# Optimization experiments

Hardware: AMD Instinct MI355X
Metric: run time of the kernel (lower is better)

## Reference

```python
import jax, jax.numpy as jnp
import numpy as np

B, L, S, H = 8, 128, 160, 768      # batch, words, wordpieces, bert hidden
T, CD = 16, 50                      # max chars per word, char embed/lstm dim
WV, WD = 50000, 100                 # word vocab, word embed dim
CV = 128                            # char vocab
NEG = -1e30


def _run_lstm(x, w_ih, w_hh, b):
    # x: [N, T, D] -> hidden states [N, T, Hc]; torch LSTM gate order i,f,g,o
    N = x.shape[0]
    Hc = w_hh.shape[1]
    def step(carry, xt):
        h, c = carry
        g = xt @ w_ih.T + h @ w_hh.T + b
        i, f, gg, o = jnp.split(g, 4, axis=-1)
        c = jax.nn.sigmoid(f) * c + jax.nn.sigmoid(i) * jnp.tanh(gg)
        h = jax.nn.sigmoid(o) * jnp.tanh(c)
        return (h, c), h
    init = (jnp.zeros((N, Hc), x.dtype), jnp.zeros((N, Hc), x.dtype))
    _, hs = jax.lax.scan(step, init, jnp.swapaxes(x, 0, 1))
    return jnp.swapaxes(hs, 0, 1)


def setup_inputs() -> dict:
    key = jax.random.key(0)
    ks = jax.random.split(key, 14)
    sc = 1.0 / np.sqrt(CD)
    return {
        "bert_emb": jax.random.normal(ks[0], (B, S, H), jnp.float32),
        "pieces2word": jax.random.randint(ks[1], (B, L, S), 0, 2, jnp.int32),
        "word_ids": jax.random.randint(ks[2], (B, L), 0, WV),
        "char_ids": jax.random.randint(ks[3], (B, L, T), 0, CV),
        "char_count": jax.random.randint(ks[4], (B, L), 0, T, jnp.int32),
        "token_masks_char": jax.random.randint(ks[5], (B, L, T), 0, 2, jnp.int32),
        "word_table": jax.random.normal(ks[6], (WV, WD), jnp.float32) * 0.02,
        "char_table": jax.random.normal(ks[7], (CV, CD), jnp.float32) * 0.02,
        "w_ih_f": jax.random.uniform(ks[8], (4 * CD, CD), jnp.float32, -sc, sc),
        "w_hh_f": jax.random.uniform(ks[9], (4 * CD, CD), jnp.float32, -sc, sc),
        "b_f": jax.random.uniform(ks[10], (4 * CD,), jnp.float32, -sc, sc),
        "w_ih_b": jax.random.uniform(ks[11], (4 * CD, CD), jnp.float32, -sc, sc),
        "w_hh_b": jax.random.uniform(ks[12], (4 * CD, CD), jnp.float32, -sc, sc),
        "b_b": jax.random.uniform(ks[13], (4 * CD,), jnp.float32, -sc, sc),
    }


def reference(bert_emb, pieces2word, word_ids, char_ids, char_count,
              token_masks_char, word_table, char_table,
              w_ih_f, w_hh_f, b_f, w_ih_b, w_hh_b, b_b):
    cls_embedding = bert_emb[:, 0]                      # [B, H]
    # piece -> word max pooling (masked fill with global min, then max)
    min_value = jax.lax.stop_gradient(jnp.min(bert_emb))
    expanded = jnp.where(pieces2word[:, :, :, None] != 0,
                         bert_emb[:, None, :, :], min_value)  # [B, L, S, H]
    word_reps = jnp.max(expanded, axis=2)               # [B, L, H]

    # word embedding lookup (emb_dropout is identity in eval)
    word_embed = word_table[word_ids]                   # [B, L, WD]

    # char biLSTM
    N = B * L
    lengths = jnp.maximum(char_count.reshape(N), 1)     # char_count[==0] = 1
    x = char_table[char_ids.reshape(N, T)]              # [N, T, CD]
    h_fwd = _run_lstm(x, w_ih_f, w_hh_f, b_f)           # [N, T, CD]
    # reverse each sequence by its true length (packed-sequence semantics)
    t = jnp.arange(T)
    rev_idx = lengths[:, None] - 1 - t[None, :]         # [N, T]
    valid = (rev_idx >= 0).astype(x.dtype)[:, :, None]
    gidx = jnp.clip(rev_idx, 0, T - 1)[:, :, None]
    x_rev = jnp.take_along_axis(x, gidx, axis=1) * valid
    h_rev = _run_lstm(x_rev, w_ih_b, w_hh_b, b_b)
    h_bwd = jnp.take_along_axis(h_rev, gidx, axis=1) * valid  # un-reverse + zero pad
    char_h = jnp.concatenate([h_fwd, h_bwd], axis=-1).reshape(B, L, T, 2 * CD)

    # combine(..., 'max'): additive -1e30 mask, max over chars, zero all-masked
    m = jnp.where(token_masks_char[:, :, :, None] == 0, NEG, 0.0).astype(char_h.dtype)
    h_token_char = jnp.max(m + char_h, axis=2)
    h_token_char = jnp.where(h_token_char == NEG, 0.0, h_token_char)  # [B, L, 2CD]

    embeds = jnp.concatenate([word_reps, word_embed, h_token_char], axis=-1)
    return embeds, cls_embedding
```

## Files before the change

kernel.cpp:

```cpp
#include <hip/hip_runtime.h>

#define B_   8
#define L_   128
#define S_   160
#define H_   768
#define T_   16
#define CD_  50
#define WD_  100
#define NGATE 200
#define NEGV (-1e30f)
#define FMAXV 3.402823466e+38f
#define NELEM (B_ * S_ * H_)

typedef short  s16x8 __attribute__((ext_vector_type(8)));
typedef float  f32x4 __attribute__((ext_vector_type(4)));

__device__ __forceinline__ unsigned short f2bf(float f) {
    unsigned u = __float_as_uint(f);
    u = (u + 0x7FFFu + ((u >> 16) & 1u)) >> 16;
    return (unsigned short)u;
}
__device__ __forceinline__ float sigm(float x) {
    return __fdividef(1.f, 1.f + __expf(-x));
}
__device__ __forceinline__ float tanh_fast(float x) {
    float a = fabsf(x);
    float e = __expf(-2.f * a);
    float t = __fdividef(1.f - e, 1.f + e);
    return copysignf(t, x);
}
__device__ __forceinline__ float4 fmax4(float4 a, float4 b) {
    return make_float4(fmaxf(a.x, b.x), fmaxf(a.y, b.y), fmaxf(a.z, b.z), fmaxf(a.w, b.w));
}

struct LstmS {
    s16x8 xall[T_][128];
    s16x8 hbuf[2][128];
    int   slen[16], smask[16];
};
struct WordS {
    int list[S_ + 8];
    int cnt;
    float red[256];
};
#define SMEM_BYTES 37120

__device__ void lstm_body(int unit, char* smem,
        const int* __restrict__ char_ids, const int* __restrict__ char_count,
        const int* __restrict__ tok_mask, const float* __restrict__ char_table,
        const float* __restrict__ w_ih_f, const float* __restrict__ w_hh_f,
        const float* __restrict__ b_f,
        const float* __restrict__ w_ih_b, const float* __restrict__ w_hh_b,
        const float* __restrict__ b_b,
        float* __restrict__ out) {
    LstmS& sh = *(LstmS*)smem;
    const int dir  = unit >> 6;
    const int grp  = unit & 63;
    const int tid  = threadIdx.x;
    const int lane = tid & 63;
    const int wv   = tid >> 6;

    if (tid < 16) {
        int n = grp * 16 + tid;
        int c = char_count[n];
        sh.slen[tid] = (c > 0) ? c : 1;
        int mb = 0;
        for (int t = 0; t < T_; ++t) mb |= (tok_mask[n * T_ + t] != 0) << t;
        sh.smask[tid] = mb;
    }
    { s16x8 z = {0,0,0,0,0,0,0,0};
      if (tid < 128) sh.hbuf[0][tid] = z; else sh.hbuf[1][tid - 128] = z; }

    const int m   = lane & 3;
    const int k2  = (lane >> 2) & 3;
    const int q   = lane >> 4;
    const int sstar = q * 4 + m;

    const float* WI = dir ? w_ih_b : w_ih_f;
    const float* WH = dir ? w_hh_b : w_hh_f;
    const float* BV = dir ? b_b    : b_f;
    const int cnt = (wv == 0) ? 4 : 3;
    int   ccol[4];
    int   cvld[4];
    int   hofs[4];
    s16x8 bf[4][4];
#pragma unroll
    for (int i = 0; i < 4; ++i) {
        int nt = (i < 3) ? (wv + 4 * i) : 12;
        int c  = nt * 4 + k2;
        int jv = (i < cnt) && (c < 50);
        ccol[i] = c;
        cvld[i] = jv;
        hofs[i] = ((c >> 3) * 16 + sstar) * 8 + (c & 7);
        int orow = m * 50 + c;
        const float* wi = WI + orow * CD_;
        const float* wh = WH + orow * CD_;
#pragma unroll
        for (int kt = 0; kt < 4; ++kt) {
            int kst = kt * 32 + q * 8;
            s16x8 fr = {0,0,0,0,0,0,0,0};
#pragma unroll
            for (int e = 0; e < 8; ++e) {
                int k = kst + e;
                float v = 0.f;
                if (jv) {
                    if (k < 64) {
                        if (k < CD_) v = wi[k];
                        else if (k == 63) v = BV[orow];
                    } else {
                        int kk = k - 64;
                        if (kk < CD_) v = wh[kk];
                    }
                }
                fr[e] = (short)f2bf(v);
            }
            bf[i][kt] = fr;
        }
    }
    __syncthreads();

    for (int idx = tid; idx < T_ * 128; idx += 256) {
        int t = idx >> 7;
        int u = idx & 127;
        int g = u >> 4, s = u & 15;
        int st = dir ? (sh.slen[s] - 1 - t) : t;
        s16x8 fr = {0,0,0,0,0,0,0,0};
        if (st >= 0) {
            int cidv = char_ids[(grp * 16 + s) * T_ + st];
            const float* row = char_table + cidv * CD_;
            int kbase = g * 8;
#pragma unroll
            for (int e = 0; e < 8; ++e) {
                int k = kbase + e;
                if (k < CD_) fr[e] = (short)f2bf(row[k]);
            }
        }
        if (g == 7) fr[7] = (short)0x3F80;
        sh.xall[t][u] = fr;
    }

    const int laneofs = (q << 4) + (lane & 15);
    const int sl_s = sh.slen[sstar];
    const int sm_s = sh.smask[sstar];

    int sms = 0;
#pragma unroll
    for (int t = 0; t < T_; ++t) {
        int tt = dir ? (sl_s - 1 - t) : t;
        if (tt >= 0 && ((sm_s >> tt) & 1)) sms |= 1 << t;
    }

    float cst0 = 0.f, cst1 = 0.f, cst2 = 0.f, cst3 = 0.f;
    float mr0 = NEGV, mr1 = NEGV, mr2 = NEGV, mr3 = NEGV;
    const bool m0 = (lane & 1) != 0;
    const bool m1 = (lane & 2) != 0;

    __syncthreads();

#define TRUPD(I, D) { \
    float v0 = (D)[0], v1 = (D)[1], v2 = (D)[2], v3 = (D)[3]; \
    float s10 = __shfl_xor(v0, 1), s11 = __shfl_xor(v1, 1); \
    float s12 = __shfl_xor(v2, 1), s13 = __shfl_xor(v3, 1); \
    float A0 = m0 ? s11 : v0; \
    float A1 = m0 ? v1 : s10; \
    float A2 = m0 ? s13 : v2; \
    float A3 = m0 ? v3 : s12; \
    float s20 = __shfl_xor(A0, 2), s21 = __shfl_xor(A1, 2); \
    float s22 = __shfl_xor(A2, 2), s23 = __shfl_xor(A3, 2); \
    float gi = m1 ? s22 : A0; \
    float gf = m1 ? s23 : A1; \
    float gg = m1 ? A2 : s20; \
    float go = m1 ? A3 : s21; \
    float cc = sigm(gf) * cst##I + sigm(gi) * tanh_fast(gg); \
    float h  = sigm(go) * tanh_fast(cc); \
    if (cvld[I]) { \
        cst##I = cc; \
        hw[hofs[I]] = f2bf(h); \
        if ((sms >> t) & 1) mr##I = fmaxf(mr##I, h); \
    } }

    __builtin_amdgcn_s_setprio(1);

#pragma unroll 1
    for (int t = 0; t < T_; ++t) {
        const int cur = t & 1, nxt = cur ^ 1;
        unsigned short* hw = (unsigned short*)&sh.hbuf[nxt][0];
        const s16x8* xb = sh.xall[t];
        s16x8 a0 = xb[laneofs];
        s16x8 a1 = xb[64 + laneofs];
        s16x8 a2 = sh.hbuf[cur][laneofs];
        s16x8 a3 = sh.hbuf[cur][64 + laneofs];

        {
            f32x4 d0 = {0.f, 0.f, 0.f, 0.f};
            f32x4 d1 = {0.f, 0.f, 0.f, 0.f};
            d0 = __builtin_amdgcn_mfma_f32_16x16x32_bf16(a0, bf[0][0], d0, 0, 0, 0);
            d1 = __builtin_amdgcn_mfma_f32_16x16x32_bf16(a0, bf[1][0], d1, 0, 0, 0);
            d0 = __builtin_amdgcn_mfma_f32_16x16x32_bf16(a1, bf[0][1], d0, 0, 0, 0);
            d1 = __builtin_amdgcn_mfma_f32_16x16x32_bf16(a1, bf[1][1], d1, 0, 0, 0);
            d0 = __builtin_amdgcn_mfma_f32_16x16x32_bf16(a2, bf[0][2], d0, 0, 0, 0);
            d1 = __builtin_amdgcn_mfma_f32_16x16x32_bf16(a2, bf[1][2], d1, 0, 0, 0);
            d0 = __builtin_amdgcn_mfma_f32_16x16x32_bf16(a3, bf[0][3], d0, 0, 0, 0);
            d1 = __builtin_amdgcn_mfma_f32_16x16x32_bf16(a3, bf[1][3], d1, 0, 0, 0);
            TRUPD(0, d0)
            TRUPD(1, d1)
        }
        {
            f32x4 d2 = {0.f, 0.f, 0.f, 0.f};
            d2 = __builtin_amdgcn_mfma_f32_16x16x32_bf16(a0, bf[2][0], d2, 0, 0, 0);
            d2 = __builtin_amdgcn_mfma_f32_16x16x32_bf16(a1, bf[2][1], d2, 0, 0, 0);
            d2 = __builtin_amdgcn_mfma_f32_16x16x32_bf16(a2, bf[2][2], d2, 0, 0, 0);
            d2 = __builtin_amdgcn_mfma_f32_16x16x32_bf16(a3, bf[2][3], d2, 0, 0, 0);
            TRUPD(2, d2)
            if (cnt == 4) {
                f32x4 d3 = {0.f, 0.f, 0.f, 0.f};
                d3 = __builtin_amdgcn_mfma_f32_16x16x32_bf16(a0, bf[3][0], d3, 0, 0, 0);
                d3 = __builtin_amdgcn_mfma_f32_16x16x32_bf16(a1, bf[3][1], d3, 0, 0, 0);
                d3 = __builtin_amdgcn_mfma_f32_16x16x32_bf16(a2, bf[3][2], d3, 0, 0, 0);
                d3 = __builtin_amdgcn_mfma_f32_16x16x32_bf16(a3, bf[3][3], d3, 0, 0, 0);
                TRUPD(3, d3)
            }
        }
        __syncthreads();
    }

    __builtin_amdgcn_s_setprio(0);

    float* ob = out + (size_t)(grp * 16 + sstar) * 968 + 868 + dir * CD_;
#define OUTW(I) if (cvld[I]) { \
    float mm = mr##I; \
    if (dir && (sm_s >> sl_s)) mm = fmaxf(mm, 0.f); \
    if (mm == NEGV) mm = 0.f; \
    ob[ccol[I]] = mm; }
    OUTW(0) OUTW(1) OUTW(2) OUTW(3)
}

__device__ void word_body(int bl, char* smem,
        const float* __restrict__ bert, const int* __restrict__ p2w,
        const int* __restrict__ word_ids, const float* __restrict__ word_table,
        float* __restrict__ out) {
    WordS& sh = *(WordS*)smem;
    int b = bl >> 7;
    int l = bl & 127;
    int tid = threadIdx.x;

    if (tid == 0) sh.cnt = 0;
    __syncthreads();
    if (tid < S_) {
        if (p2w[bl * S_ + tid]) {
            int p = atomicAdd(&sh.cnt, 1);
            sh.list[p] = tid;
        }
    }
    __syncthreads();
    int n = sh.cnt;

    float* orow = out + (size_t)bl * 968;

    if (n > 0) {
        if (tid < ((8 - (n & 7)) & 7)) sh.list[n + tid] = sh.list[0];
        __syncthreads();
        int n8 = (n + 7) & ~7;
        if (tid < 192) {
            const float4* bb = (const float4*)(bert + (size_t)b * S_ * H_) + tid;
            float4 mx = make_float4(-FMAXV, -FMAXV, -FMAXV, -FMAXV);
            for (int i = 0; i < n8; i += 8) {
                float4 v0 = bb[(size_t)sh.list[i]     * 192];
                float4 v1 = bb[(size_t)sh.list[i + 1] * 192];
                float4 v2 = bb[(size_t)sh.list[i + 2] * 192];
                float4 v3 = bb[(size_t)sh.list[i + 3] * 192];
                float4 v4 = bb[(size_t)sh.list[i + 4] * 192];
                float4 v5 = bb[(size_t)sh.list[i + 5] * 192];
                float4 v6 = bb[(size_t)sh.list[i + 6] * 192];
                float4 v7 = bb[(size_t)sh.list[i + 7] * 192];
                mx = fmax4(mx, fmax4(fmax4(fmax4(v0, v1), fmax4(v2, v3)),
                                     fmax4(fmax4(v4, v5), fmax4(v6, v7))));
            }
            ((float4*)orow)[tid] = mx;
        } else {
            int j = tid - 192;
            int wid = word_ids[bl];
            orow[768 + j] = word_table[(size_t)wid * WD_ + j];
            if (j < WD_ - 64) orow[768 + 64 + j] = word_table[(size_t)wid * WD_ + 64 + j];
        }
    } else {
        float mv = FMAXV;
        const float4* x4 = (const float4*)bert;
        for (int i = tid; i < NELEM / 4; i += 256) {
            float4 v = x4[i];
            mv = fminf(mv, fminf(fminf(v.x, v.y), fminf(v.z, v.w)));
        }
        sh.red[tid] = mv;
        __syncthreads();
        for (int o = 128; o > 0; o >>= 1) {
            if (tid < o) sh.red[tid] = fminf(sh.red[tid], sh.red[tid + o]);
            __syncthreads();
        }
        float g = sh.red[0];
        if (tid < 192) {
            ((float4*)orow)[tid] = make_float4(g, g, g, g);
        } else {
            int j = tid - 192;
            int wid = word_ids[bl];
            orow[768 + j] = word_table[(size_t)wid * WD_ + j];
            if (j < WD_ - 64) orow[768 + 64 + j] = word_table[(size_t)wid * WD_ + 64 + j];
        }
    }

    if (l == 0 && tid < 192) {
        const float4* c4 = (const float4*)(bert + (size_t)b * S_ * H_);
        float4* co = (float4*)(out + (size_t)B_ * L_ * 968 + (size_t)b * H_);
        co[tid] = c4[tid];
    }
}

__global__ __launch_bounds__(256, 1) void kmega(
        const float* __restrict__ bert, const int* __restrict__ p2w,
        const int* __restrict__ word_ids, const int* __restrict__ char_ids,
        const int* __restrict__ char_count, const int* __restrict__ tok_mask,
        const float* __restrict__ word_table, const float* __restrict__ char_table,
        const float* __restrict__ w_ih_f, const float* __restrict__ w_hh_f,
        const float* __restrict__ b_f,
        const float* __restrict__ w_ih_b, const float* __restrict__ w_hh_b,
        const float* __restrict__ b_b,
        float* __restrict__ out) {
    __shared__ __align__(16) char smem[SMEM_BYTES];
    int bid = blockIdx.x;
    if (bid < 128) {
        lstm_body(bid, smem, char_ids, char_count, tok_mask, char_table,
                  w_ih_f, w_hh_f, b_f, w_ih_b, w_hh_b, b_b, out);
    } else {
        word_body(bid - 128, smem, bert, p2w, word_ids, word_table, out);
    }
}

extern "C" void kernel_launch(void* const* d_in, const int* in_sizes, int n_in,
                              void* d_out, int out_size, void* d_ws, size_t ws_size,
                              hipStream_t stream) {
    const float* bert       = (const float*)d_in[0];
    const int*   p2w        = (const int*)d_in[1];
    const int*   word_ids   = (const int*)d_in[2];
    const int*   char_ids   = (const int*)d_in[3];
    const int*   char_count = (const int*)d_in[4];
    const int*   tok_mask   = (const int*)d_in[5];
    const float* word_table = (const float*)d_in[6];
    const float* char_table = (const float*)d_in[7];
    const float* w_ih_f = (const float*)d_in[8];
    const float* w_hh_f = (const float*)d_in[9];
    const float* b_f    = (const float*)d_in[10];
    const float* w_ih_b = (const float*)d_in[11];
    const float* w_hh_b = (const float*)d_in[12];
    const float* b_b    = (const float*)d_in[13];

    float* out = (float*)d_out;

    kmega<<<128 + B_ * L_, 256, 0, stream>>>(bert, p2w, word_ids, char_ids, char_count, tok_mask,
                                             word_table, char_table,
                                             w_ih_f, w_hh_f, b_f, w_ih_b, w_hh_b, b_b, out);
}
```

Baseline: 45.15 us.

## Use 512-thread blocks: spread LSTM column tiles over 8 waves, pair words per block

Block size goes from 256 to 512 threads. In the LSTM blocks, each of the 8 waves now owns at most two 16-column gate tiles instead of up to four, which halves the serial MFMA and activation work per wave in each recurrent step. The word blocks now process two words each, and the grid shrinks to 640 blocks. The costs are heavier barrier synchronisation across 8 waves per timestep, and the all-zero-word fallback now uses a serial 256-element min loop instead of a tree reduction.

```diff
diff --git a/kernel.cpp b/kernel.cpp
--- a/kernel.cpp
+++ b/kernel.cpp
@@ -38,10 +38,10 @@
     s16x8 hbuf[2][128];
     int   slen[16], smask[16];
 };
-struct WordS {
-    int list[S_ + 8];
-    int cnt;
-    float red[256];
+struct Word2S {
+    int   list[2][S_ + 8];
+    int   cnt[2];
+    float red[2][256];
 };
 #define SMEM_BYTES 37120
 
@@ -68,8 +68,7 @@
         for (int t = 0; t < T_; ++t) mb |= (tok_mask[n * T_ + t] != 0) << t;
         sh.smask[tid] = mb;
     }
-    { s16x8 z = {0,0,0,0,0,0,0,0};
-      if (tid < 128) sh.hbuf[0][tid] = z; else sh.hbuf[1][tid - 128] = z; }
+    if (tid < 256) { s16x8 z = {0,0,0,0,0,0,0,0}; ((s16x8*)sh.hbuf)[tid] = z; }
 
     const int m   = lane & 3;
     const int k2  = (lane >> 2) & 3;
@@ -79,47 +78,52 @@
     const float* WI = dir ? w_ih_b : w_ih_f;
     const float* WH = dir ? w_hh_b : w_hh_f;
     const float* BV = dir ? b_b    : b_f;
-    const int cnt = (wv == 0) ? 4 : 3;
-    int   ccol[4];
-    int   cvld[4];
-    int   hofs[4];
-    s16x8 bf[4][4];
-#pragma unroll
-    for (int i = 0; i < 4; ++i) {
-        int nt = (i < 3) ? (wv + 4 * i) : 12;
-        int c  = nt * 4 + k2;
-        int jv = (i < cnt) && (c < 50);
-        ccol[i] = c;
-        cvld[i] = jv;
-        hofs[i] = ((c >> 3) * 16 + sstar) * 8 + (c & 7);
-        int orow = m * 50 + c;
-        const float* wi = WI + orow * CD_;
-        const float* wh = WH + orow * CD_;
-#pragma unroll
-        for (int kt = 0; kt < 4; ++kt) {
-            int kst = kt * 32 + q * 8;
-            s16x8 fr = {0,0,0,0,0,0,0,0};
-#pragma unroll
-            for (int e = 0; e < 8; ++e) {
-                int k = kst + e;
-                float v = 0.f;
-                if (jv) {
-                    if (k < 64) {
-                        if (k < CD_) v = wi[k];
-                        else if (k == 63) v = BV[orow];
-                    } else {
-                        int kk = k - 64;
-                        if (kk < CD_) v = wh[kk];
-                    }
-                }
-                fr[e] = (short)f2bf(v);
-            }
-            bf[i][kt] = fr;
-        }
-    }
-    __syncthreads();
-
-    for (int idx = tid; idx < T_ * 128; idx += 256) {
+
+    const int  ntA = wv;
+    const int  ntB = 8 + wv;
+    const bool hasB = (wv < 5);
+    const int  cA = ntA * 4 + k2;
+    const int  cB = ntB * 4 + k2;
+    const bool vB = hasB && (cB < CD_);
+    const int  hofsA = ((cA >> 3) * 16 + sstar) * 8 + (cA & 7);
+    const int  hofsB = ((cB >> 3) * 16 + sstar) * 8 + (cB & 7);
+
+#define LDFRAG(FR, OROW, KT, VALID) { \
+    s16x8 fr_ = {0,0,0,0,0,0,0,0}; \
+    if (VALID) { \
+        const float* wi_ = WI + (OROW) * CD_; \
+        const float* wh_ = WH + (OROW) * CD_; \
+        int kst_ = (KT) * 32 + q * 8; \
+        _Pragma("unroll") \
+        for (int e = 0; e < 8; ++e) { \
+            int k = kst_ + e; \
+            float v = 0.f; \
+            if (k < 64) { \
+                if (k < CD_) v = wi_[k]; \
+                else if (k == 63) v = BV[OROW]; \
+            } else { \
+                int kk = k - 64; \
+                if (kk < CD_) v = wh_[kk]; \
+            } \
+            fr_[e] = (short)f2bf(v); \
+        } \
+    } \
+    FR = fr_; }
+
+    const int orowA = m * 50 + cA;
+    const int orowB = m * 50 + ((cB < CD_) ? cB : 0);
+    s16x8 bfA0, bfA1, bfA2, bfA3, bfB0, bfB1, bfB2, bfB3;
+    LDFRAG(bfA0, orowA, 0, true)
+    LDFRAG(bfA1, orowA, 1, true)
+    LDFRAG(bfA2, orowA, 2, true)
+    LDFRAG(bfA3, orowA, 3, true)
+    LDFRAG(bfB0, orowB, 0, vB)
+    LDFRAG(bfB1, orowB, 1, vB)
+    LDFRAG(bfB2, orowB, 2, vB)
+    LDFRAG(bfB3, orowB, 3, vB)
+    __syncthreads();
+
+    for (int idx = tid; idx < T_ * 128; idx += 512) {
         int t = idx >> 7;
         int u = idx & 127;
         int g = u >> 4, s = u & 15;
@@ -150,14 +154,14 @@
         if (tt >= 0 && ((sm_s >> tt) & 1)) sms |= 1 << t;
     }
 
-    float cst0 = 0.f, cst1 = 0.f, cst2 = 0.f, cst3 = 0.f;
-    float mr0 = NEGV, mr1 = NEGV, mr2 = NEGV, mr3 = NEGV;
+    float cstA = 0.f, cstB = 0.f;
+    float mrA = NEGV, mrB = NEGV;
     const bool m0 = (lane & 1) != 0;
     const bool m1 = (lane & 2) != 0;
 
     __syncthreads();
 
-#define TRUPD(I, D) { \
+#define TRUPD(VLD, HOF, CST, MR, D) { \
     float v0 = (D)[0], v1 = (D)[1], v2 = (D)[2], v3 = (D)[3]; \
     float s10 = __shfl_xor(v0, 1), s11 = __shfl_xor(v1, 1); \
     float s12 = __shfl_xor(v2, 1), s13 = __shfl_xor(v3, 1); \
@@ -171,12 +175,12 @@
     float gf = m1 ? s23 : A1; \
     float gg = m1 ? A2 : s20; \
     float go = m1 ? A3 : s21; \
-    float cc = sigm(gf) * cst##I + sigm(gi) * tanh_fast(gg); \
+    float cc = sigm(gf) * (CST) + sigm(gi) * tanh_fast(gg); \
     float h  = sigm(go) * tanh_fast(cc); \
-    if (cvld[I]) { \
-        cst##I = cc; \
-        hw[hofs[I]] = f2bf(h); \
-        if ((sms >> t) & 1) mr##I = fmaxf(mr##I, h); \
+    if (VLD) { \
+        CST = cc; \
+        hw[HOF] = f2bf(h); \
+        if ((sms >> t) & 1) MR = fmaxf(MR, h); \
     } }
 
     __builtin_amdgcn_s_setprio(1);
@@ -193,33 +197,19 @@
 
         {
             f32x4 d0 = {0.f, 0.f, 0.f, 0.f};
+            d0 = __builtin_amdgcn_mfma_f32_16x16x32_bf16(a0, bfA0, d0, 0, 0, 0);
+            d0 = __builtin_amdgcn_mfma_f32_16x16x32_bf16(a1, bfA1, d0, 0, 0, 0);
+            d0 = __builtin_amdgcn_mfma_f32_16x16x32_bf16(a2, bfA2, d0, 0, 0, 0);
+            d0 = __builtin_amdgcn_mfma_f32_16x16x32_bf16(a3, bfA3, d0, 0, 0, 0);
+            TRUPD(true, hofsA, cstA, mrA, d0)
+        }
+        if (hasB) {
             f32x4 d1 = {0.f, 0.f, 0.f, 0.f};
-            d0 = __builtin_amdgcn_mfma_f32_16x16x32_bf16(a0, bf[0][0], d0, 0, 0, 0);
-            d1 = __builtin_amdgcn_mfma_f32_16x16x32_bf16(a0, bf[1][0], d1, 0, 0, 0);
-            d0 = __builtin_amdgcn_mfma_f32_16x16x32_bf16(a1, bf[0][1], d0, 0, 0, 0);
-            d1 = __builtin_amdgcn_mfma_f32_16x16x32_bf16(a1, bf[1][1], d1, 0, 0, 0);
-            d0 = __builtin_amdgcn_mfma_f32_16x16x32_bf16(a2, bf[0][2], d0, 0, 0, 0);
-            d1 = __builtin_amdgcn_mfma_f32_16x16x32_bf16(a2, bf[1][2], d1, 0, 0, 0);
-            d0 = __builtin_amdgcn_mfma_f32_16x16x32_bf16(a3, bf[0][3], d0, 0, 0, 0);
-            d1 = __builtin_amdgcn_mfma_f32_16x16x32_bf16(a3, bf[1][3], d1, 0, 0, 0);
-            TRUPD(0, d0)
-            TRUPD(1, d1)
-        }
-        {
-            f32x4 d2 = {0.f, 0.f, 0.f, 0.f};
-            d2 = __builtin_amdgcn_mfma_f32_16x16x32_bf16(a0, bf[2][0], d2, 0, 0, 0);
-            d2 = __builtin_amdgcn_mfma_f32_16x16x32_bf16(a1, bf[2][1], d2, 0, 0, 0);
-            d2 = __builtin_amdgcn_mfma_f32_16x16x32_bf16(a2, bf[2][2], d2, 0, 0, 0);
-            d2 = __builtin_amdgcn_mfma_f32_16x16x32_bf16(a3, bf[2][3], d2, 0, 0, 0);
-            TRUPD(2, d2)
-            if (cnt == 4) {
-                f32x4 d3 = {0.f, 0.f, 0.f, 0.f};
-                d3 = __builtin_amdgcn_mfma_f32_16x16x32_bf16(a0, bf[3][0], d3, 0, 0, 0);
-                d3 = __builtin_amdgcn_mfma_f32_16x16x32_bf16(a1, bf[3][1], d3, 0, 0, 0);
-                d3 = __builtin_amdgcn_mfma_f32_16x16x32_bf16(a2, bf[3][2], d3, 0, 0, 0);
-                d3 = __builtin_amdgcn_mfma_f32_16x16x32_bf16(a3, bf[3][3], d3, 0, 0, 0);
-                TRUPD(3, d3)
-            }
+            d1 = __builtin_amdgcn_mfma_f32_16x16x32_bf16(a0, bfB0, d1, 0, 0, 0);
+            d1 = __builtin_amdgcn_mfma_f32_16x16x32_bf16(a1, bfB1, d1, 0, 0, 0);
+            d1 = __builtin_amdgcn_mfma_f32_16x16x32_bf16(a2, bfB2, d1, 0, 0, 0);
+            d1 = __builtin_amdgcn_mfma_f32_16x16x32_bf16(a3, bfB3, d1, 0, 0, 0);
+            TRUPD(vB, hofsB, cstB, mrB, d1)
         }
         __syncthreads();
     }
@@ -227,94 +217,107 @@
     __builtin_amdgcn_s_setprio(0);
 
     float* ob = out + (size_t)(grp * 16 + sstar) * 968 + 868 + dir * CD_;
-#define OUTW(I) if (cvld[I]) { \
-    float mm = mr##I; \
-    if (dir && (sm_s >> sl_s)) mm = fmaxf(mm, 0.f); \
-    if (mm == NEGV) mm = 0.f; \
-    ob[ccol[I]] = mm; }
-    OUTW(0) OUTW(1) OUTW(2) OUTW(3)
-}
-
-__device__ void word_body(int bl, char* smem,
+    {
+        float mm = mrA;
+        if (dir && (sm_s >> sl_s)) mm = fmaxf(mm, 0.f);
+        if (mm == NEGV) mm = 0.f;
+        ob[cA] = mm;
+    }
+    if (vB) {
+        float mm = mrB;
+        if (dir && (sm_s >> sl_s)) mm = fmaxf(mm, 0.f);
+        if (mm == NEGV) mm = 0.f;
+        ob[cB] = mm;
+    }
+}
+
+__device__ void word_body2(int blk, char* smem,
         const float* __restrict__ bert, const int* __restrict__ p2w,
         const int* __restrict__ word_ids, const float* __restrict__ word_table,
         float* __restrict__ out) {
-    WordS& sh = *(WordS*)smem;
-    int b = bl >> 7;
-    int l = bl & 127;
-    int tid = threadIdx.x;
-
-    if (tid == 0) sh.cnt = 0;
-    __syncthreads();
-    if (tid < S_) {
-        if (p2w[bl * S_ + tid]) {
-            int p = atomicAdd(&sh.cnt, 1);
-            sh.list[p] = tid;
-        }
-    }
-    __syncthreads();
-    int n = sh.cnt;
+    Word2S& sh = *(Word2S*)smem;
+    const int tid = threadIdx.x;
+    const int h   = tid >> 8;
+    const int lid = tid & 255;
+    const int bl  = blk * 2 + h;
+    const int b   = bl >> 7;
+    const int l   = bl & 127;
+
+    if (lid == 0) sh.cnt[h] = 0;
+    __syncthreads();
+    if (lid < S_) {
+        if (p2w[bl * S_ + lid]) {
+            int p = atomicAdd(&sh.cnt[h], 1);
+            sh.list[h][p] = lid;
+        }
+    }
+    __syncthreads();
+    const int n = sh.cnt[h];
+    if (n > 0 && lid < ((8 - (n & 7)) & 7)) sh.list[h][n + lid] = sh.list[h][0];
+    __syncthreads();
+
+    float gmin = 0.f;
+    if (n == 0) {
+        float mv = FMAXV;
+        const float4* x4 = (const float4*)bert;
+        for (int i = lid; i < NELEM / 4; i += 256) {
+            float4 v = x4[i];
+            mv = fminf(mv, fminf(fminf(v.x, v.y), fminf(v.z, v.w)));
+        }
+        sh.red[h][lid] = mv;
+    }
+    __syncthreads();
+    if (n == 0) {
+        float g = FMAXV;
+        for (int k = 0; k < 256; ++k) g = fminf(g, sh.red[h][k]);
+        gmin = g;
+    }
 
     float* orow = out + (size_t)bl * 968;
-
     if (n > 0) {
-        if (tid < ((8 - (n & 7)) & 7)) sh.list[n + tid] = sh.list[0];
-        __syncthreads();
         int n8 = (n + 7) & ~7;
-        if (tid < 192) {
-            const float4* bb = (const float4*)(bert + (size_t)b * S_ * H_) + tid;
+        if (lid < 192) {
+            const float4* bb = (const float4*)(bert + (size_t)b * S_ * H_) + lid;
             float4 mx = make_float4(-FMAXV, -FMAXV, -FMAXV, -FMAXV);
+            const int* lst = sh.list[h];
             for (int i = 0; i < n8; i += 8) {
-                float4 v0 = bb[(size_t)sh.list[i]     * 192];
-                float4 v1 = bb[(size_t)sh.list[i + 1] * 192];
-                float4 v2 = bb[(size_t)sh.list[i + 2] * 192];
-                float4 v3 = bb[(size_t)sh.list[i + 3] * 192];
-                float4 v4 = bb[(size_t)sh.list[i + 4] * 192];
-                float4 v5 = bb[(size_t)sh.list[i + 5] * 192];
-                float4 v6 = bb[(size_t)sh.list[i + 6] * 192];
-                float4 v7 = bb[(size_t)sh.list[i + 7] * 192];
+                float4 v0 = bb[(size_t)lst[i]     * 192];
+                float4 v1 = bb[(size_t)lst[i + 1] * 192];
+                float4 v2 = bb[(size_t)lst[i + 2] * 192];
+                float4 v3 = bb[(size_t)lst[i + 3] * 192];
+                float4 v4 = bb[(size_t)lst[i + 4] * 192];
+                float4 v5 = bb[(size_t)lst[i + 5] * 192];
+                float4 v6 = bb[(size_t)lst[i + 6] * 192];
+                float4 v7 = bb[(size_t)lst[i + 7] * 192];
                 mx = fmax4(mx, fmax4(fmax4(fmax4(v0, v1), fmax4(v2, v3)),
                                      fmax4(fmax4(v4, v5), fmax4(v6, v7))));
             }
-            ((float4*)orow)[tid] = mx;
+            ((float4*)orow)[lid] = mx;
         } else {
-            int j = tid - 192;
+            int j = lid - 192;
             int wid = word_ids[bl];
             orow[768 + j] = word_table[(size_t)wid * WD_ + j];
             if (j < WD_ - 64) orow[768 + 64 + j] = word_table[(size_t)wid * WD_ + 64 + j];
         }
     } else {
-        float mv = FMAXV;
-        const float4* x4 = (const float4*)bert;
-        for (int i = tid; i < NELEM / 4; i += 256) {
-            float4 v = x4[i];
-            mv = fminf(mv, fminf(fminf(v.x, v.y), fminf(v.z, v.w)));
-        }
-        sh.red[tid] = mv;
-        __syncthreads();
-        for (int o = 128; o > 0; o >>= 1) {
-            if (tid < o) sh.red[tid] = fminf(sh.red[tid], sh.red[tid + o]);
-            __syncthreads();
-        }
-        float g = sh.red[0];
-        if (tid < 192) {
-            ((float4*)orow)[tid] = make_float4(g, g, g, g);
+        if (lid < 192) {
+            ((float4*)orow)[lid] = make_float4(gmin, gmin, gmin, gmin);
         } else {
-            int j = tid - 192;
+            int j = lid - 192;
             int wid = word_ids[bl];
             orow[768 + j] = word_table[(size_t)wid * WD_ + j];
             if (j < WD_ - 64) orow[768 + 64 + j] = word_table[(size_t)wid * WD_ + 64 + j];
         }
     }
 
-    if (l == 0 && tid < 192) {
+    if (l == 0 && lid < 192) {
         const float4* c4 = (const float4*)(bert + (size_t)b * S_ * H_);
         float4* co = (float4*)(out + (size_t)B_ * L_ * 968 + (size_t)b * H_);
-        co[tid] = c4[tid];
-    }
-}
-
-__global__ __launch_bounds__(256, 1) void kmega(
+        co[lid] = c4[lid];
+    }
+}
+
+__global__ __launch_bounds__(512, 2) void kmega(
         const float* __restrict__ bert, const int* __restrict__ p2w,
         const int* __restrict__ word_ids, const int* __restrict__ char_ids,
         const int* __restrict__ char_count, const int* __restrict__ tok_mask,
@@ -330,7 +333,7 @@
         lstm_body(bid, smem, char_ids, char_count, tok_mask, char_table,
                   w_ih_f, w_hh_f, b_f, w_ih_b, w_hh_b, b_b, out);
     } else {
-        word_body(bid - 128, smem, bert, p2w, word_ids, word_table, out);
+        word_body2(bid - 128, smem, bert, p2w, word_ids, word_table, out);
     }
 }
 
@@ -354,7 +357,7 @@
 
     float* out = (float*)d_out;
 
-    kmega<<<128 + B_ * L_, 256, 0, stream>>>(bert, p2w, word_ids, char_ids, char_count, tok_mask,
-                                             word_table, char_table,
-                                             w_ih_f, w_hh_f, b_f, w_ih_b, w_hh_b, b_b, out);
-}
+    kmega<<<128 + 512, 512, 0, stream>>>(bert, p2w, word_ids, char_ids, char_count, tok_mask,
+                                         word_table, char_table,
+                                         w_ih_f, w_hh_f, b_f, w_ih_b, w_hh_b, b_b, out);
+}
```

After: 40.21 us. 1.12x faster.
